# Kernel tuning notes

Hardware: AMD Instinct MI355X
Metric: run time of the kernel (lower is better)

The kernel has to match this reference:

```python
import jax, jax.numpy as jnp
import numpy as np

B, S, H = 1, 2048, 2048
NH, NKV, HD = 16, 4, 128
N_REP = NH // NKV
WINDOW = 1024
THETA = 10000.0


def _rope(x, fc):
    # x: [B,S,h,HD]; fc: [B,S,HD//2,2] (cos,sin)
    xr = x.reshape(*x.shape[:-1], HD // 2, 2)
    a, b = xr[..., 0], xr[..., 1]
    cos = fc[:, :, None, :, 0]
    sin = fc[:, :, None, :, 1]
    out = jnp.stack((a * cos - b * sin, a * sin + b * cos), axis=-1)
    return out.reshape(x.shape)


def setup_inputs() -> dict:
    key = jax.random.key(0)
    ks = jax.random.split(key, 5)
    hidden_state = jax.random.normal(ks[0], (B, S, H), jnp.float32)
    # rotary table: cos/sin of pos * theta^{-2i/d}
    inv_freq = 1.0 / (THETA ** (jnp.arange(0, HD, 2, dtype=jnp.float32) / HD))
    ang = jnp.arange(S, dtype=jnp.float32)[:, None] * inv_freq[None, :]  # [S, HD//2]
    freq_cis = jnp.stack((jnp.cos(ang), jnp.sin(ang)), axis=-1)  # [S, HD//2, 2]
    attention_mask = jnp.ones((B, S), dtype=bool)
    i = jnp.arange(S)[:, None]
    j = jnp.arange(S)[None, :]
    causal_mask = ((j <= i) & (i - j < WINDOW))[None, None]  # [1,1,S,S] sliding-window causal
    position_ids = jnp.broadcast_to(jnp.arange(S, dtype=jnp.int32), (B, S))
    scale = 0.02
    Wq = jax.random.normal(ks[1], (H, NH * HD), jnp.float32) * scale
    Wk = jax.random.normal(ks[2], (H, NKV * HD), jnp.float32) * scale
    Wv = jax.random.normal(ks[3], (H, NKV * HD), jnp.float32) * scale
    Wo = jax.random.normal(ks[4], (NH * HD, H), jnp.float32) * scale
    return {"hidden_state": hidden_state, "freq_cis": freq_cis,
            "attention_mask": attention_mask, "causal_mask": causal_mask,
            "position_ids": position_ids, "Wq": Wq, "Wk": Wk, "Wv": Wv, "Wo": Wo}


def reference(hidden_state, freq_cis, attention_mask, causal_mask, position_ids,
              Wq, Wk, Wv, Wo):
    q = (hidden_state @ Wq).reshape(B, S, NH, HD)
    k = (hidden_state @ Wk).reshape(B, S, NKV, HD)
    v = (hidden_state @ Wv).reshape(B, S, NKV, HD)
    fc = freq_cis[position_ids]  # [B,S,HD//2,2]
    q = _rope(q, fc)
    k = _rope(k, fc)
    # GQA: repeat kv heads (contiguous groups, as in repeat_kv)
    k = jnp.repeat(k, N_REP, axis=2)  # [B,S,NH,HD]
    v = jnp.repeat(v, N_REP, axis=2)
    mask = causal_mask & attention_mask[:, None, None, :]  # [B,1,S,S]
    bias = jnp.where(mask, 0.0, jnp.finfo(jnp.float32).min)
    scores = jnp.einsum('bqhd,bkhd->bhqk', q, k) * (1.0 / np.sqrt(HD))
    attn = jax.nn.softmax(scores + bias, axis=-1)
    out = jnp.einsum('bhqk,bkhd->bqhd', attn, v).reshape(B, S, NH * HD)
    return out @ Wo
```

## Files before the change

kernel.cpp:

```cpp
#include <hip/hip_runtime.h>
#include <hip/hip_bf16.h>
#include <stdint.h>

#define S_LEN 2048
#define HDIM  2048
#define NHQ   16
#define NKVH  4
#define HD    128
#define WIN   1024
#define SM_SCALE 0.08838834764831845f
#define NEG_BIG  -1.0e30f

typedef __attribute__((ext_vector_type(8))) short short8;
typedef __attribute__((ext_vector_type(4))) float float4v;
typedef unsigned short u16;

static __device__ __forceinline__ float bf2f(u16 u) {
  union { unsigned int i; float f; } v; v.i = ((unsigned int)u) << 16; return v.f;
}
static __device__ __forceinline__ u16 f2bf(float f) {
  union { float f; unsigned int i; } v; v.f = f;
  unsigned int x = v.i;
  return (u16)((x + 0x7fffu + ((x >> 16) & 1u)) >> 16);
}

__global__ __launch_bounds__(256) void prep(
    const float* __restrict__ hs, const float* __restrict__ Wq,
    const float* __restrict__ Wk, const float* __restrict__ Wv,
    const float* __restrict__ Wo, u16* __restrict__ hsB,
    u16* __restrict__ WqkvT, u16* __restrict__ WoT)
{
  const int b = blockIdx.x;
  if (b < 1024) {
    u16* dst = hsB + (size_t)b * 4096;
    const int mb = b >> 6, ks = b & 63;
#pragma unroll
    for (int i = 0; i < 2; ++i) {
      const int cid = i * 256 + threadIdx.x;
      const int kc  = cid & 3;
      const int m   = cid >> 2;
      const float* src = hs + ((size_t)(mb * 128 + m)) * 2048 + ks * 32 + kc * 8;
      const float4 v0 = *(const float4*)src;
      const float4 v1 = *(const float4*)(src + 4);
      short8 o;
      o[0] = (short)f2bf(v0.x); o[1] = (short)f2bf(v0.y);
      o[2] = (short)f2bf(v0.z); o[3] = (short)f2bf(v0.w);
      o[4] = (short)f2bf(v1.x); o[5] = (short)f2bf(v1.y);
      o[6] = (short)f2bf(v1.z); o[7] = (short)f2bf(v1.w);
      *(short8*)(dst + (kc * 128 + m) * 8) = o;
    }
    return;
  }

  __shared__ u16 t[32][33];
  const int tx = threadIdx.x & 31, ty = threadIdx.x >> 5;
  int n0, kstep;
  const float* W; u16* DT; int nsrc, N;
  if (b < 7168) {
    const int bb = b - 1024;
    n0    = (bb % 96) * 32;
    kstep = bb / 96;
    if (n0 < 2048)      { W = Wq; nsrc = n0;        N = 2048; }
    else if (n0 < 2560) { W = Wk; nsrc = n0 - 2048; N = 512;  }
    else                { W = Wv; nsrc = n0 - 2560; N = 512;  }
    DT = WqkvT;
  } else {
    const int bb = b - 7168;
    n0    = (bb & 63) * 32;
    kstep = bb >> 6;
    W = Wo; nsrc = n0; N = 2048; DT = WoT;
  }
  const int k0 = kstep * 32;

#pragma unroll
  for (int i = 0; i < 4; ++i)
    t[ty + i * 8][tx] = f2bf(W[(size_t)(k0 + ty + i * 8) * N + nsrc + tx]);
  __syncthreads();
  const int kc = tx >> 3, e = tx & 7;
#pragma unroll
  for (int i = 0; i < 4; ++i) {
    const int n = n0 + ty + i * 8;
    DT[((size_t)((n >> 6) * 64 + kstep)) * 2048 + kc * 512 + (n & 63) * 8 + e]
        = t[tx][ty + i * 8];
  }
}

template <int EPI>
__global__ __launch_bounds__(256) void gemm_bt(
    const u16* __restrict__ Apk, const u16* __restrict__ Bpk,
    void* __restrict__ Cv, const float* __restrict__ fc,
    u16* __restrict__ Qb, u16* __restrict__ Kp, u16* __restrict__ Vp,
    int M, int N, int K)
{
  __shared__ u16 Als[2][8192];
  __shared__ u16 Bls[2][4096];

  const int tid  = threadIdx.x;
  const int lane = tid & 63;
  const int w    = tid >> 6;
  const int quad = lane >> 4;
  const int lc   = lane & 15;
  const int n0   = blockIdx.x * 64;
  const int m0   = blockIdx.y * 128;
  const int wr   = (w >> 1) * 64;
  const int wc   = (w & 1) * 32;
  const int ktiles = K >> 5;
  const int nk2    = ktiles >> 1;

  const char* aB = (const char*)(Apk + (size_t)(m0 >> 7) * ktiles * 4096);
  const char* bB = (const char*)(Bpk + (size_t)(n0 >> 6) * ktiles * 2048);

  float4v acc[4][2];
#pragma unroll
  for (int i = 0; i < 4; ++i)
#pragma unroll
    for (int j = 0; j < 2; ++j) acc[i][j] = (float4v){0.f, 0.f, 0.f, 0.f};

  auto stage = [&](int bi, int kk) {
    const char* ab = aB + (size_t)kk * 16384;
    const char* bb = bB + (size_t)kk * 8192;
#pragma unroll
    for (int r = 0; r < 4; ++r) {
      const int off = r * 4096 + tid * 16;
      __builtin_amdgcn_global_load_lds(
          (__attribute__((address_space(1))) void*)(ab + off),
          (__attribute__((address_space(3))) void*)((char*)Als[bi] + off), 16, 0, 0);
    }
#pragma unroll
    for (int r = 0; r < 2; ++r) {
      const int off = r * 4096 + tid * 16;
      __builtin_amdgcn_global_load_lds(
          (__attribute__((address_space(1))) void*)(bb + off),
          (__attribute__((address_space(3))) void*)((char*)Bls[bi] + off), 16, 0, 0);
    }
  };

  stage(0, 0);
  __syncthreads();
  int cur = 0;
  for (int kk = 0; kk < nk2; ++kk) {
    if (kk + 1 < nk2) stage(cur ^ 1, kk + 1);
#pragma unroll
    for (int half = 0; half < 2; ++half) {
      const u16* Ab = Als[cur] + half * 4096;
      const u16* Bb = Bls[cur] + half * 2048;
      short8 af[4], bfr[2];
#pragma unroll
      for (int mi = 0; mi < 4; ++mi)
        af[mi] = *(const short8*)(Ab + quad * 1024 + (wr + mi * 16 + lc) * 8);
#pragma unroll
      for (int ni = 0; ni < 2; ++ni)
        bfr[ni] = *(const short8*)(Bb + quad * 512 + (wc + ni * 16 + lc) * 8);
#pragma unroll
      for (int mi = 0; mi < 4; ++mi)
#pragma unroll
        for (int ni = 0; ni < 2; ++ni)
          acc[mi][ni] = __builtin_amdgcn_mfma_f32_16x16x32_bf16(
              af[mi], bfr[ni], acc[mi][ni], 0, 0, 0);
    }
    __syncthreads();
    cur ^= 1;
  }

  if (EPI == 0) {
#pragma unroll
    for (int mi = 0; mi < 4; ++mi)
#pragma unroll
      for (int ni = 0; ni < 2; ++ni)
#pragma unroll
        for (int r = 0; r < 4; ++r) {
          const int row = m0 + wr + mi * 16 + quad * 4 + r;
          const int col = n0 + wc + ni * 16 + lc;
          ((float*)Cv)[(size_t)row * N + col] = acc[mi][ni][r];
        }
  } else {
    if (n0 < 2560) {
#pragma unroll
      for (int mi = 0; mi < 4; ++mi)
#pragma unroll
        for (int ni = 0; ni < 2; ++ni)
#pragma unroll
          for (int r = 0; r < 4; ++r) {
            const int row = m0 + wr + mi * 16 + quad * 4 + r;
            const int col = n0 + wc + ni * 16 + lc;
            const int hh  = col & 127;
            const float v = acc[mi][ni][r];
            const float p = __shfl_xor(v, 1);
            const float2 cs = *(const float2*)(fc + row * 128 + (hh & ~1));
            const float res = (col & 1) ? (p * cs.y + v * cs.x)
                                        : (v * cs.x - p * cs.y);
            if (n0 < 2048) {
              Qb[(size_t)row * 2048 + col] = f2bf(res);
            } else {
              const int kvh = (col - 2048) >> 7;
              const int kt  = row >> 6, key = row & 63;
              const int ks   = hh >> 5;
              const int qd   = (hh >> 3) & 3;
              const int e    = hh & 7;
              const int ntk  = key >> 4;
              const int lck  = key & 15;
              Kp[((size_t)(kvh * 32 + kt)) * 8192
                 + ((ks * 4 + ntk) << 9) + ((qd * 16 + lck) << 3) + e] = f2bf(res);
            }
          }
    } else {
#pragma unroll
      for (int mi = 0; mi < 4; ++mi)
#pragma unroll
        for (int ni = 0; ni < 2; ++ni)
#pragma unroll
          for (int r = 0; r < 4; ++r) {
            const int row = m0 + wr + mi * 16 + quad * 4 + r;
            const int col = n0 + wc + ni * 16 + lc;
            const int kvh = (col - 2560) >> 7;
            const int hd  = col & 127;
            const int kt  = row >> 6, key = row & 63;
            const int ktk  = (key >> 5) & 1;
            const int qd   = (key >> 3) & 3;
            const int e    = key & 7;
            const int nt2  = hd >> 4;
            const int lcv  = hd & 15;
            Vp[((size_t)(kvh * 32 + kt)) * 8192
               + ((ktk * 8 + nt2) << 9) + ((qd * 16 + lcv) << 3) + e]
                = f2bf(acc[mi][ni][r]);
          }
    }
  }
}

__global__ __launch_bounds__(64, 3) void attn_kernel(
    const u16* __restrict__ Qb, const u16* __restrict__ kp,
    const u16* __restrict__ vp, u16* __restrict__ out)
{
  __shared__ u16 P[16 * 72];

  const int lane = threadIdx.x;
  const int quad = lane >> 4;
  const int lc   = lane & 15;

  const int id = blockIdx.x;
  const int u  = id & 255;
  const int g  = id >> 8;
  const int h  = u & 15;
  const int w  = (u >> 4) & 3;
  const int j2 = u >> 6;
  const int t  = g * 4 + j2;
  const int kvh = h >> 2;
  const int rb  = t * 64 + w * 16;

  short8 qf[4];
  {
    const u16* qp = Qb + (size_t)(rb + lc) * 2048 + h * HD + quad * 8;
#pragma unroll
    for (int ks = 0; ks < 4; ++ks) qf[ks] = *(const short8*)(qp + ks * 32);
  }

  float4v o[8];
#pragma unroll
  for (int i = 0; i < 8; ++i) o[i] = (float4v){0.f, 0.f, 0.f, 0.f};
  float mrow[4], lrow[4];
#pragma unroll
  for (int r = 0; r < 4; ++r) { mrow[r] = NEG_BIG; lrow[r] = 0.f; }

  int jmin = rb - (WIN - 1); if (jmin < 0) jmin = 0;
  const int kt_begin = jmin >> 6;
  const int kt_end   = (rb + 15) >> 6;

  const size_t tbase = (size_t)(kvh * 32) * 8192;
  const int lofs = lane << 3;

  for (int kt = kt_begin; kt <= kt_end; ++kt) {
    const int k0 = kt * 64;
    const u16* kg = kp + tbase + (size_t)kt * 8192;
    const u16* vg = vp + tbase + (size_t)kt * 8192;

    float4v sacc[4];
#pragma unroll
    for (int i = 0; i < 4; ++i) sacc[i] = (float4v){0.f, 0.f, 0.f, 0.f};
    __builtin_amdgcn_s_setprio(1);
#pragma unroll
    for (int ks = 0; ks < 4; ++ks) {
#pragma unroll
      for (int nt = 0; nt < 4; ++nt) {
        short8 kb = *(const short8*)(kg + ((ks * 4 + nt) << 9) + lofs);
        sacc[nt] = __builtin_amdgcn_mfma_f32_16x16x32_bf16(qf[ks], kb, sacc[nt], 0, 0, 0);
      }
    }
    __builtin_amdgcn_s_setprio(0);

    const bool full = (k0 + 63 <= rb) && ((rb + 15 - k0) <= WIN - 1);
    float sv[4][4];
    float rmax[4] = {NEG_BIG, NEG_BIG, NEG_BIG, NEG_BIG};
    if (full) {
#pragma unroll
      for (int nt = 0; nt < 4; ++nt)
#pragma unroll
        for (int r = 0; r < 4; ++r) {
          const float sx = sacc[nt][r] * SM_SCALE;
          sv[nt][r] = sx;
          rmax[r] = fmaxf(rmax[r], sx);
        }
    } else {
#pragma unroll
      for (int nt = 0; nt < 4; ++nt) {
        const int j = k0 + nt * 16 + lc;
#pragma unroll
        for (int r = 0; r < 4; ++r) {
          const int i = rb + quad * 4 + r;
          const bool valid = (j <= i) && (i - j < WIN);
          const float sx = valid ? sacc[nt][r] * SM_SCALE : NEG_BIG;
          sv[nt][r] = sx;
          rmax[r] = fmaxf(rmax[r], sx);
        }
      }
    }
#pragma unroll
    for (int off = 1; off < 16; off <<= 1)
#pragma unroll
      for (int r = 0; r < 4; ++r)
        rmax[r] = fmaxf(rmax[r], __shfl_xor(rmax[r], off, 64));

    bool grow = false;
#pragma unroll
    for (int r = 0; r < 4; ++r) grow |= (rmax[r] > mrow[r]);
    if (__any((int)grow)) {
#pragma unroll
      for (int r = 0; r < 4; ++r) {
        const float mn = fmaxf(mrow[r], rmax[r]);
        const float a  = __expf(mrow[r] - mn);
        mrow[r] = mn;
        lrow[r] *= a;
#pragma unroll
        for (int i = 0; i < 8; ++i) o[i][r] *= a;
      }
    }

    float rsum[4] = {0.f, 0.f, 0.f, 0.f};
#pragma unroll
    for (int nt = 0; nt < 4; ++nt)
#pragma unroll
      for (int r = 0; r < 4; ++r) {
        const float p = __expf(sv[nt][r] - mrow[r]);
        rsum[r] += p;
        P[(quad * 4 + r) * 72 + nt * 16 + lc] = f2bf(p);
      }
#pragma unroll
    for (int off = 1; off < 16; off <<= 1)
#pragma unroll
      for (int r = 0; r < 4; ++r)
        rsum[r] += __shfl_xor(rsum[r], off, 64);
#pragma unroll
    for (int r = 0; r < 4; ++r) lrow[r] += rsum[r];

    __builtin_amdgcn_s_setprio(1);
#pragma unroll
    for (int ktk = 0; ktk < 2; ++ktk) {
      short8 pa = *(const short8*)(P + lc * 72 + ktk * 32 + quad * 8);
#pragma unroll
      for (int nt2 = 0; nt2 < 8; ++nt2) {
        short8 vb = *(const short8*)(vg + ((ktk * 8 + nt2) << 9) + lofs);
        o[nt2] = __builtin_amdgcn_mfma_f32_16x16x32_bf16(pa, vb, o[nt2], 0, 0, 0);
      }
    }
    __builtin_amdgcn_s_setprio(0);
  }

#pragma unroll
  for (int r = 0; r < 4; ++r) {
    const float inv = (lrow[r] > 0.f) ? (1.f / lrow[r]) : 0.f;
    const int row = rb + quad * 4 + r;
    const size_t mbase = (size_t)(row >> 7) * 64;
    const int m = row & 127;
#pragma unroll
    for (int nt2 = 0; nt2 < 8; ++nt2) {
      const int col = h * HD + nt2 * 16 + lc;
      const int kstep = col >> 5, kc = (col >> 3) & 3, e = col & 7;
      out[(mbase + kstep) * 4096 + kc * 1024 + m * 8 + e] = f2bf(o[nt2][r] * inv);
    }
  }
}

extern "C" void kernel_launch(void* const* d_in, const int* in_sizes, int n_in,
                              void* d_out, int out_size, void* d_ws, size_t ws_size,
                              hipStream_t stream) {
  const float* hs = (const float*)d_in[0];
  const float* fc = (const float*)d_in[1];
  const float* Wq = (const float*)d_in[5];
  const float* Wk = (const float*)d_in[6];
  const float* Wv = (const float*)d_in[7];
  const float* Wo = (const float*)d_in[8];
  float* outp = (float*)d_out;

  u16* hsB   = (u16*)d_ws;
  u16* WqkvT = hsB   + (size_t)2048 * 2048;
  u16* WoT   = WqkvT + (size_t)3072 * 2048;
  u16* Qb    = WoT   + (size_t)2048 * 2048;
  u16* ATTN  = Qb    + (size_t)2048 * 2048;
  u16* Kp    = ATTN  + (size_t)2048 * 2048;
  u16* Vp    = Kp    + (size_t)4 * 2048 * 128;

  dim3 blk(256);
  prep<<<dim3(11264), blk, 0, stream>>>(hs, Wq, Wk, Wv, Wo, hsB, WqkvT, WoT);
  gemm_bt<1><<<dim3(3072 / 64, 2048 / 128), blk, 0, stream>>>(
      hsB, WqkvT, nullptr, fc, Qb, Kp, Vp, 2048, 3072, 2048);
  attn_kernel<<<dim3(2048), dim3(64), 0, stream>>>(Qb, Kp, Vp, ATTN);
  gemm_bt<0><<<dim3(2048 / 64, 2048 / 128), blk, 0, stream>>>(
      ATTN, WoT, outp, nullptr, nullptr, nullptr, nullptr, 2048, 2048, 2048);
}
```

Measured before the change: 253.2 us.

## Prefetch next K tile and current V tile into registers in attention loop

The attention kernel now loads the whole K tile for the next key block into registers while softmax runs, and issues all V loads for the current block at the start of the iteration, so global-load latency overlaps with the MFMA and exp work. This takes many more VGPRs, so the launch bound is lowered from 3 to 2 waves per SIMD, and the score buffer is reused in place to save registers. The cost is lower occupancy and less latency hiding across waves.

```diff
diff --git a/kernel.cpp b/kernel.cpp
--- a/kernel.cpp
+++ b/kernel.cpp
@@ -228,7 +228,7 @@
   }
 }
 
-__global__ __launch_bounds__(64, 3) void attn_kernel(
+__global__ __launch_bounds__(64, 2) void attn_kernel(
     const u16* __restrict__ Qb, const u16* __restrict__ kp,
     const u16* __restrict__ vp, u16* __restrict__ out)
 {
@@ -269,27 +269,49 @@
   const size_t tbase = (size_t)(kvh * 32) * 8192;
   const int lofs = lane << 3;
 
+  short8 ka[8], kb8[8];
+  {
+    const u16* kg = kp + tbase + (size_t)kt_begin * 8192;
+#pragma unroll
+    for (int i = 0; i < 8; ++i) ka[i]  = *(const short8*)(kg + (i << 9) + lofs);
+#pragma unroll
+    for (int i = 0; i < 8; ++i) kb8[i] = *(const short8*)(kg + ((8 + i) << 9) + lofs);
+  }
+
   for (int kt = kt_begin; kt <= kt_end; ++kt) {
     const int k0 = kt * 64;
-    const u16* kg = kp + tbase + (size_t)kt * 8192;
-    const u16* vg = vp + tbase + (size_t)kt * 8192;
+
+    short8 va[8], vb8[8];
+    {
+      const u16* vg = vp + tbase + (size_t)kt * 8192;
+#pragma unroll
+      for (int i = 0; i < 8; ++i) va[i]  = *(const short8*)(vg + (i << 9) + lofs);
+#pragma unroll
+      for (int i = 0; i < 8; ++i) vb8[i] = *(const short8*)(vg + ((8 + i) << 9) + lofs);
+    }
 
     float4v sacc[4];
 #pragma unroll
     for (int i = 0; i < 4; ++i) sacc[i] = (float4v){0.f, 0.f, 0.f, 0.f};
     __builtin_amdgcn_s_setprio(1);
 #pragma unroll
-    for (int ks = 0; ks < 4; ++ks) {
-#pragma unroll
-      for (int nt = 0; nt < 4; ++nt) {
-        short8 kb = *(const short8*)(kg + ((ks * 4 + nt) << 9) + lofs);
-        sacc[nt] = __builtin_amdgcn_mfma_f32_16x16x32_bf16(qf[ks], kb, sacc[nt], 0, 0, 0);
-      }
+    for (int nt = 0; nt < 4; ++nt) {
+      sacc[nt] = __builtin_amdgcn_mfma_f32_16x16x32_bf16(qf[0], ka[nt],      sacc[nt], 0, 0, 0);
+      sacc[nt] = __builtin_amdgcn_mfma_f32_16x16x32_bf16(qf[1], ka[4 + nt],  sacc[nt], 0, 0, 0);
+      sacc[nt] = __builtin_amdgcn_mfma_f32_16x16x32_bf16(qf[2], kb8[nt],     sacc[nt], 0, 0, 0);
+      sacc[nt] = __builtin_amdgcn_mfma_f32_16x16x32_bf16(qf[3], kb8[4 + nt], sacc[nt], 0, 0, 0);
     }
     __builtin_amdgcn_s_setprio(0);
 
+    if (kt < kt_end) {
+      const u16* kg = kp + tbase + (size_t)(kt + 1) * 8192;
+#pragma unroll
+      for (int i = 0; i < 8; ++i) ka[i]  = *(const short8*)(kg + (i << 9) + lofs);
+#pragma unroll
+      for (int i = 0; i < 8; ++i) kb8[i] = *(const short8*)(kg + ((8 + i) << 9) + lofs);
+    }
+
     const bool full = (k0 + 63 <= rb) && ((rb + 15 - k0) <= WIN - 1);
-    float sv[4][4];
     float rmax[4] = {NEG_BIG, NEG_BIG, NEG_BIG, NEG_BIG};
     if (full) {
 #pragma unroll
@@ -297,7 +319,7 @@
 #pragma unroll
         for (int r = 0; r < 4; ++r) {
           const float sx = sacc[nt][r] * SM_SCALE;
-          sv[nt][r] = sx;
+          sacc[nt][r] = sx;
           rmax[r] = fmaxf(rmax[r], sx);
         }
     } else {
@@ -309,7 +331,7 @@
           const int i = rb + quad * 4 + r;
           const bool valid = (j <= i) && (i - j < WIN);
           const float sx = valid ? sacc[nt][r] * SM_SCALE : NEG_BIG;
-          sv[nt][r] = sx;
+          sacc[nt][r] = sx;
           rmax[r] = fmaxf(rmax[r], sx);
         }
       }
@@ -340,7 +362,7 @@
     for (int nt = 0; nt < 4; ++nt)
 #pragma unroll
       for (int r = 0; r < 4; ++r) {
-        const float p = __expf(sv[nt][r] - mrow[r]);
+        const float p = __expf(sacc[nt][r] - mrow[r]);
         rsum[r] += p;
         P[(quad * 4 + r) * 72 + nt * 16 + lc] = f2bf(p);
       }
@@ -353,14 +375,15 @@
     for (int r = 0; r < 4; ++r) lrow[r] += rsum[r];
 
     __builtin_amdgcn_s_setprio(1);
-#pragma unroll
-    for (int ktk = 0; ktk < 2; ++ktk) {
-      short8 pa = *(const short8*)(P + lc * 72 + ktk * 32 + quad * 8);
-#pragma unroll
-      for (int nt2 = 0; nt2 < 8; ++nt2) {
-        short8 vb = *(const short8*)(vg + ((ktk * 8 + nt2) << 9) + lofs);
-        o[nt2] = __builtin_amdgcn_mfma_f32_16x16x32_bf16(pa, vb, o[nt2], 0, 0, 0);
-      }
+    {
+      short8 pa0 = *(const short8*)(P + lc * 72 + quad * 8);
+#pragma unroll
+      for (int nt2 = 0; nt2 < 8; ++nt2)
+        o[nt2] = __builtin_amdgcn_mfma_f32_16x16x32_bf16(pa0, va[nt2], o[nt2], 0, 0, 0);
+      short8 pa1 = *(const short8*)(P + lc * 72 + 32 + quad * 8);
+#pragma unroll
+      for (int nt2 = 0; nt2 < 8; ++nt2)
+        o[nt2] = __builtin_amdgcn_mfma_f32_16x16x32_bf16(pa1, vb8[nt2], o[nt2], 0, 0, 0);
     }
     __builtin_amdgcn_s_setprio(0);
   }
```

After: 224.9 us. -11.2%, faster.
